# Performance work log

Measured on AMD Instinct MI355X. Metric: run time of the kernel, lower is better.

The kernel has to match this reference:

```python
import jax, jax.numpy as jnp
import numpy as np

B, S, HID, NH, INTER, VOCAB = 8, 1024, 512, 8, 2048, 30522
EPS = 1e-12


def _layernorm(x, w, b):
    m = jnp.mean(x, axis=-1, keepdims=True)
    v = jnp.mean((x - m) ** 2, axis=-1, keepdims=True)
    return (x - m) * jax.lax.rsqrt(v + EPS) * w + b


def _multihead_mut(x, M):
    # x: (b, s, d); M: (H, s, s). Split d into H heads, mix along the
    # sequence axis per head: out[b,t,h,d] = sum_s x[b,s,h,d] * M[h,s,t]
    b, s, d = x.shape
    xh = x.reshape(b, s, NH, d // NH)
    out = jnp.einsum('bshd,hst->bthd', xh, M)
    return out.reshape(b, s, d)


def setup_inputs() -> dict:
    key = jax.random.key(0)
    ks = jax.random.split(key, 14)
    g = lambda i, shape, scale: jax.random.normal(ks[i], shape, dtype=jnp.float32) * scale
    return {
        'x': jax.random.randint(ks[0], (B, S), 0, VOCAB),
        'word_emb': g(1, (VOCAB, HID), 0.02),
        'pos_emb': g(2, (S, HID), 0.02),
        'tok_emb': g(3, (2, HID), 0.02),
        'emb_ln_w': jnp.ones((HID,), dtype=jnp.float32),
        'emb_ln_b': jnp.zeros((HID,), dtype=jnp.float32),
        'init_d': g(4, (INTER, HID), 0.02),
        'init_b': g(5, (INTER,), 0.02),
        'init_M': g(6, (NH, S, S), 1.0 / np.sqrt(S)),
        'inter0_d': g(7, (INTER, INTER), 1.0 / np.sqrt(INTER)),
        'inter0_b': g(8, (INTER,), 0.02),
        'inter0_M': g(9, (NH, S, S), 1.0 / np.sqrt(S)),
        'final_d': g(10, (HID, INTER), 1.0 / np.sqrt(INTER)),
        'final_b': g(11, (HID,), 0.02),
    }


def reference(x, word_emb, pos_emb, tok_emb, emb_ln_w, emb_ln_b,
              init_d, init_b, init_M, inter0_d, inter0_b, inter0_M,
              final_d, final_b):
    # BertEmbeddings: word + position + token_type(all zeros) -> LayerNorm
    emb = word_emb[x] + pos_emb[None, :, :] + tok_emb[0][None, None, :]
    xo = _layernorm(emb, emb_ln_w, emb_ln_b)  # (B, S, HID)

    # layer 0 (flattened): project to intermediate, per-head seq mix, bias, quad act
    xo = xo @ init_d.T                      # (B, S, INTER)
    xo = _multihead_mut(xo, init_M)
    xo = xo + init_b
    xo = xo * xo                            # activation_quad

    # layer 1 (flattened)
    xo = xo @ inter0_d.T                    # (B, S, INTER)
    xo = _multihead_mut(xo, inter0_M)
    xo = xo + inter0_b
    xo = xo * xo                            # activation_quad

    return xo @ final_d.T + final_b         # (B, S, HID)
```

## Files before the change

kernel.cpp:

```cpp
#include <hip/hip_runtime.h>

typedef _Float16 f16;
typedef _Float16 f16x4 __attribute__((ext_vector_type(4)));
typedef _Float16 f16x8 __attribute__((ext_vector_type(8)));
typedef float    f32x4 __attribute__((ext_vector_type(4)));

#define SEQ   1024
#define HID   512
#define NHEAD 8
#define DH    256
#define INTER 2048
#define BATCH 8
#define ROWS  (BATCH * SEQ)

__device__ __forceinline__ void g2l16(const void* g, void* l) {
  __builtin_amdgcn_global_load_lds(
      (const __attribute__((address_space(1))) void*)g,
      (__attribute__((address_space(3))) void*)l, 16, 0, 0);
}

__device__ __forceinline__ void mm_core256(const f16* __restrict__ At,
                                           const f16* __restrict__ Bt,
                                           int K, f32x4 (&acc)[8][4]) {
  __shared__ __align__(16) f16 As[3 * 8192];
  __shared__ __align__(16) f16 Bs[3 * 8192];
  const int tid  = threadIdx.x;
  const int lane = tid & 63, wv = tid >> 6;
  const int wrow = (wv >> 2) * 128, wcol = (wv & 3) * 64;

  const int ch0 = tid, ch1 = tid + 512;
  const int r0 = ch0 >> 2, s0 = ch0 & 3;
  const int r1 = ch1 >> 2, s1 = ch1 & 3;
  const int g0 = r0 * K + ((s0 ^ ((r0 >> 1) & 3)) << 3);
  const int g1 = r1 * K + ((s1 ^ ((r1 >> 1) & 3)) << 3);
  const int l0 = wv * 512;
  const int l1 = 4096 + wv * 512;

  int aoff[8], boff[4];
  const int q = lane >> 4;
  #pragma unroll
  for (int m = 0; m < 8; ++m) {
    int r = wrow + m * 16 + (lane & 15);
    aoff[m] = r * 32 + ((q ^ ((r >> 1) & 3)) << 3);
  }
  #pragma unroll
  for (int n = 0; n < 4; ++n) {
    int r = wcol + n * 16 + (lane & 15);
    boff[n] = r * 32 + ((q ^ ((r >> 1) & 3)) << 3);
  }

  const int nt = K >> 5;
  g2l16(At + g0, &As[l0]);
  g2l16(At + g1, &As[l1]);
  g2l16(Bt + g0, &Bs[l0]);
  g2l16(Bt + g1, &Bs[l1]);
  g2l16(At + 32 + g0, &As[8192 + l0]);
  g2l16(At + 32 + g1, &As[8192 + l1]);
  g2l16(Bt + 32 + g0, &Bs[8192 + l0]);
  g2l16(Bt + 32 + g1, &Bs[8192 + l1]);
  __builtin_amdgcn_sched_barrier(0);
  asm volatile("s_waitcnt vmcnt(4)" ::: "memory");
  __builtin_amdgcn_s_barrier();
  __builtin_amdgcn_sched_barrier(0);

  int slot = 0;
  for (int t = 0; t < nt; ++t) {
    const int cb = slot * 8192;
    const int sb = (slot == 0 ? 2 : slot - 1) * 8192;
    const bool pf = (t + 2 < nt);
    const int kpre = (t + 2) << 5;

    f16x8 bfr[4], af0[4], af1[4];
    #pragma unroll
    for (int n = 0; n < 4; ++n) bfr[n] = *(const f16x8*)&Bs[cb + boff[n]];
    #pragma unroll
    for (int m = 0; m < 4; ++m) af0[m] = *(const f16x8*)&As[cb + aoff[m]];
    if (pf) {
      g2l16(At + kpre + g0, &As[sb + l0]);
      g2l16(At + kpre + g1, &As[sb + l1]);
    }
    __builtin_amdgcn_s_setprio(1);
    #pragma unroll
    for (int m = 0; m < 4; ++m)
      #pragma unroll
      for (int n = 0; n < 4; ++n)
        acc[m][n] = __builtin_amdgcn_mfma_f32_16x16x32_f16(af0[m], bfr[n],
                                                           acc[m][n], 0, 0, 0);
    __builtin_amdgcn_s_setprio(0);
    #pragma unroll
    for (int m = 0; m < 4; ++m) af1[m] = *(const f16x8*)&As[cb + aoff[m + 4]];
    if (pf) {
      g2l16(Bt + kpre + g0, &Bs[sb + l0]);
      g2l16(Bt + kpre + g1, &Bs[sb + l1]);
    }
    __builtin_amdgcn_s_setprio(1);
    #pragma unroll
    for (int m = 0; m < 4; ++m)
      #pragma unroll
      for (int n = 0; n < 4; ++n)
        acc[m + 4][n] = __builtin_amdgcn_mfma_f32_16x16x32_f16(af1[m], bfr[n],
                                                               acc[m + 4][n], 0, 0, 0);
    __builtin_amdgcn_s_setprio(0);
    if (t + 1 < nt) {
      __builtin_amdgcn_sched_barrier(0);
      if (pf) asm volatile("s_waitcnt vmcnt(4)" ::: "memory");
      else    asm volatile("s_waitcnt vmcnt(0)" ::: "memory");
      __builtin_amdgcn_s_barrier();
      __builtin_amdgcn_sched_barrier(0);
    }
    slot = (slot == 2) ? 0 : slot + 1;
  }
}

__device__ __forceinline__ void zero_acc8(f32x4 (&acc)[8][4]) {
  f32x4 z = {0.f, 0.f, 0.f, 0.f};
  #pragma unroll
  for (int i = 0; i < 8; ++i)
    #pragma unroll
    for (int j = 0; j < 4; ++j) acc[i][j] = z;
}

__global__ __launch_bounds__(512, 2) void gemm256_t_kernel(
    const f16* __restrict__ A, const f16* __restrict__ W,
    f16* __restrict__ Xt, int K) {
  int row0 = blockIdx.y * 256, col0 = blockIdx.x * 256;
  f32x4 acc[8][4];
  zero_acc8(acc);
  mm_core256(A + (size_t)row0 * K, W + (size_t)col0 * K, K, acc);
  int tid = threadIdx.x, lane = tid & 63, wv = tid >> 6;
  int wrow = (wv >> 2) * 128, wcol = (wv & 3) * 64;
  int cn = lane & 15, rbase = (lane >> 4) * 4;
  int b = row0 >> 10, sbase = row0 & 1023;
  #pragma unroll
  for (int m = 0; m < 8; ++m) {
    int s = sbase + wrow + m * 16 + rbase;
    #pragma unroll
    for (int n = 0; n < 4; ++n) {
      int col = col0 + wcol + n * 16 + cn;
      int h = col >> 8, d = col & 255;
      f16x4 v = {(f16)acc[m][n][0], (f16)acc[m][n][1],
                 (f16)acc[m][n][2], (f16)acc[m][n][3]};
      *(f16x4*)&Xt[(((size_t)(b * 8 + h) * 256 + d) << 10) + s] = v;
    }
  }
}

__global__ __launch_bounds__(512, 2) void mut256_kernel(
    const f16* __restrict__ Mt, const f16* __restrict__ Xt,
    const float* __restrict__ bias, f16* __restrict__ Y) {
  int b = blockIdx.z >> 3, h = blockIdx.z & 7;
  int t0 = blockIdx.y * 256;
  f32x4 acc[8][4];
  zero_acc8(acc);
  const f16* Ap = Mt + ((size_t)h << 20) + ((size_t)t0 << 10);
  const f16* Bp = Xt + (((size_t)(b * 8 + h)) << 18);
  mm_core256(Ap, Bp, SEQ, acc);
  int tid = threadIdx.x, lane = tid & 63, wv = tid >> 6;
  int wrow = (wv >> 2) * 128, wcol = (wv & 3) * 64;
  int cn = lane & 15, rbase = (lane >> 4) * 4;
  #pragma unroll
  for (int m = 0; m < 8; ++m) {
    int t = t0 + wrow + m * 16 + rbase;
    #pragma unroll
    for (int n = 0; n < 4; ++n) {
      int d = wcol + n * 16 + cn;
      float bb = bias[(h << 8) + d];
      size_t base = (((size_t)(b << 10) + t) << 11) + (h << 8) + d;
      #pragma unroll
      for (int r = 0; r < 4; ++r) {
        float v = acc[m][n][r] + bb;
        Y[base + (size_t)r * INTER] = (f16)(v * v);
      }
    }
  }
}

__device__ __forceinline__ void mm_core(const f16* __restrict__ At,
                                        const f16* __restrict__ Bt,
                                        int K, f32x4 (&acc)[4][4]) {
  __shared__ __align__(16) f16 As[2 * 4096];
  __shared__ __align__(16) f16 Bs[2 * 4096];
  const int tid  = threadIdx.x;
  const int lane = tid & 63, wv = tid >> 6;
  const int wm = (wv >> 1) * 64, wn = (wv & 1) * 64;
  const int lrow  = lane & 15;
  const int kfrag = (lane >> 4) * 8;
  const int c0  = wv * 128 + lane;
  const int r0c = c0 >> 2, q0c = c0 & 3;
  const int c1  = c0 + 64;
  const int r1c = c1 >> 2, q1c = c1 & 3;
  const int ga0 = r0c * K + ((q0c ^ ((r0c >> 1) & 3)) << 3);
  const int ga1 = r1c * K + ((q1c ^ ((r1c >> 1) & 3)) << 3);
  f16* lA0 = &As[wv * 1024];
  f16* lA1 = &As[wv * 1024 + 512];
  f16* lB0 = &Bs[wv * 1024];
  f16* lB1 = &Bs[wv * 1024 + 512];
  int aoff[4], boff[4];
  #pragma unroll
  for (int t = 0; t < 4; ++t) {
    int ra = wm + t * 16 + lrow;
    aoff[t] = ra * 32 + (kfrag ^ (((ra >> 1) & 3) << 3));
    int rb = wn + t * 16 + lrow;
    boff[t] = rb * 32 + (kfrag ^ (((rb >> 1) & 3) << 3));
  }
  g2l16(At + ga0, lA0);
  g2l16(At + ga1, lA1);
  g2l16(Bt + ga0, lB0);
  g2l16(Bt + ga1, lB1);
  __syncthreads();
  int cur = 0;
  for (int k0 = 0; k0 < K; k0 += 32) {
    if (k0 + 32 < K) {
      const int nb = (cur ^ 1) * 4096;
      g2l16(At + (k0 + 32) + ga0, lA0 + nb);
      g2l16(At + (k0 + 32) + ga1, lA1 + nb);
      g2l16(Bt + (k0 + 32) + ga0, lB0 + nb);
      g2l16(Bt + (k0 + 32) + ga1, lB1 + nb);
    }
    const int cb = cur * 4096;
    f16x8 af[4], bf[4];
    #pragma unroll
    for (int t = 0; t < 4; ++t) {
      af[t] = *(const f16x8*)&As[cb + aoff[t]];
      bf[t] = *(const f16x8*)&Bs[cb + boff[t]];
    }
    #pragma unroll
    for (int i = 0; i < 4; ++i)
      #pragma unroll
      for (int j = 0; j < 4; ++j)
        acc[i][j] = __builtin_amdgcn_mfma_f32_16x16x32_f16(af[i], bf[j],
                                                           acc[i][j], 0, 0, 0);
    __syncthreads();
    cur ^= 1;
  }
}

__device__ __forceinline__ void zero_acc(f32x4 (&acc)[4][4]) {
  f32x4 z = {0.f, 0.f, 0.f, 0.f};
  #pragma unroll
  for (int i = 0; i < 4; ++i)
    #pragma unroll
    for (int j = 0; j < 4; ++j) acc[i][j] = z;
}

__global__ __launch_bounds__(256) void gemm_out_kernel(
    const f16* __restrict__ A, const f16* __restrict__ W,
    const float* __restrict__ bias, float* __restrict__ out, int K, int N) {
  int row0 = blockIdx.y * 128, col0 = blockIdx.x * 128;
  f32x4 acc[4][4];
  zero_acc(acc);
  mm_core(A + (size_t)row0 * K, W + (size_t)col0 * K, K, acc);
  int tid = threadIdx.x, lane = tid & 63, wv = tid >> 6;
  int wm = (wv >> 1) * 64, wn = (wv & 1) * 64;
  int cn = lane & 15, rbase = (lane >> 4) * 4;
  #pragma unroll
  for (int mt = 0; mt < 4; ++mt) {
    int r0 = row0 + wm + mt * 16 + rbase;
    #pragma unroll
    for (int nt = 0; nt < 4; ++nt) {
      int col = col0 + wn + nt * 16 + cn;
      float bb = bias[col];
      #pragma unroll
      for (int r = 0; r < 4; ++r)
        out[(size_t)(r0 + r) * N + col] = acc[mt][nt][r] + bb;
    }
  }
}

__global__ __launch_bounds__(256) void embed_ln_kernel(
    const int* __restrict__ x, const float* __restrict__ wemb,
    const float* __restrict__ pemb, const float* __restrict__ temb,
    const float* __restrict__ lnw, const float* __restrict__ lnb,
    f16* __restrict__ out) {
  int row = blockIdx.x;
  int s = row & (SEQ - 1);
  int tok = x[row];
  const float* we = wemb + (size_t)tok * HID;
  const float* pe = pemb + (size_t)s * HID;
  int c = threadIdx.x;
  float e0 = we[c] + pe[c] + temb[c];
  float e1 = we[c + 256] + pe[c + 256] + temb[c + 256];
  float s1 = e0 + e1, s2 = e0 * e0 + e1 * e1;
  #pragma unroll
  for (int off = 32; off > 0; off >>= 1) {
    s1 += __shfl_down(s1, off, 64);
    s2 += __shfl_down(s2, off, 64);
  }
  __shared__ float r1[4], r2[4];
  int wid = threadIdx.x >> 6, lane = threadIdx.x & 63;
  if (lane == 0) { r1[wid] = s1; r2[wid] = s2; }
  __syncthreads();
  float S1 = r1[0] + r1[1] + r1[2] + r1[3];
  float S2 = r2[0] + r2[1] + r2[2] + r2[3];
  float m = S1 * (1.0f / HID);
  float v = S2 * (1.0f / HID) - m * m;
  float inv = rsqrtf(v + 1e-12f);
  f16* o = out + (size_t)row * HID;
  o[c]       = (f16)((e0 - m) * inv * lnw[c]       + lnb[c]);
  o[c + 256] = (f16)((e1 - m) * inv * lnw[c + 256] + lnb[c + 256]);
}

__global__ __launch_bounds__(256) void cast_f16_kernel(
    const float* __restrict__ in, f16* __restrict__ out, int n) {
  int i = (blockIdx.x * 256 + threadIdx.x) * 4;
  if (i < n) {
    float4 v = *(const float4*)(in + i);
    f16x4 o = {(f16)v.x, (f16)v.y, (f16)v.z, (f16)v.w};
    *(f16x4*)(out + i) = o;
  }
}

__global__ __launch_bounds__(256) void mtrans_kernel(
    const float* __restrict__ M, f16* __restrict__ Mt) {
  __shared__ float T[32][33];
  int h = blockIdx.z;
  int s0 = blockIdx.y * 32, t0 = blockIdx.x * 32;
  int tx = threadIdx.x & 31, ty = threadIdx.x >> 5;
  const float* Mh = M + ((size_t)h << 20);
  #pragma unroll
  for (int i = 0; i < 32; i += 8)
    T[ty + i][tx] = Mh[((size_t)(s0 + ty + i) << 10) + t0 + tx];
  __syncthreads();
  f16* Mth = Mt + ((size_t)h << 20);
  #pragma unroll
  for (int i = 0; i < 32; i += 8)
    Mth[((size_t)(t0 + ty + i) << 10) + s0 + tx] = (f16)T[tx][ty + i];
}

extern "C" void kernel_launch(void* const* d_in, const int* in_sizes, int n_in,
                              void* d_out, int out_size, void* d_ws, size_t ws_size,
                              hipStream_t stream) {
  const int*   x        = (const int*)d_in[0];
  const float* wemb     = (const float*)d_in[1];
  const float* pemb     = (const float*)d_in[2];
  const float* temb     = (const float*)d_in[3];
  const float* lnw      = (const float*)d_in[4];
  const float* lnb      = (const float*)d_in[5];
  const float* init_d   = (const float*)d_in[6];
  const float* init_b   = (const float*)d_in[7];
  const float* init_M   = (const float*)d_in[8];
  const float* inter0_d = (const float*)d_in[9];
  const float* inter0_b = (const float*)d_in[10];
  const float* inter0_M = (const float*)d_in[11];
  const float* final_d  = (const float*)d_in[12];
  const float* final_b  = (const float*)d_in[13];
  float* out = (float*)d_out;

  char* ws = (char*)d_ws;
  f16* R0 = (f16*)(ws);
  f16* R1 = (f16*)(ws + 8388608);
  f16* R2 = (f16*)(ws + 10485760);
  f16* R3 = (f16*)(ws + 27262976);
  f16* R4 = (f16*)(ws + 60817408);
  f16* R5 = (f16*)(ws + 94371840);

  embed_ln_kernel<<<ROWS, 256, 0, stream>>>(x, wemb, pemb, temb, lnw, lnb, R0);
  cast_f16_kernel<<<(INTER * HID / 4 + 255) / 256, 256, 0, stream>>>(init_d, R1, INTER * HID);
  mtrans_kernel<<<dim3(32, 32, 8), 256, 0, stream>>>(init_M, R2);
  gemm256_t_kernel<<<dim3(INTER / 256, ROWS / 256), 512, 0, stream>>>(R0, R1, R3, HID);
  mut256_kernel<<<dim3(1, SEQ / 256, BATCH * NHEAD), 512, 0, stream>>>(R2, R3, init_b, R4);
  cast_f16_kernel<<<(INTER * INTER / 4 + 255) / 256, 256, 0, stream>>>(inter0_d, R0, INTER * INTER);
  mtrans_kernel<<<dim3(32, 32, 8), 256, 0, stream>>>(inter0_M, R2);
  gemm256_t_kernel<<<dim3(INTER / 256, ROWS / 256), 512, 0, stream>>>(R4, R0, R5, INTER);
  mut256_kernel<<<dim3(1, SEQ / 256, BATCH * NHEAD), 512, 0, stream>>>(R2, R5, inter0_b, R3);
  cast_f16_kernel<<<(HID * INTER / 4 + 255) / 256, 256, 0, stream>>>(final_d, R1, HID * INTER);
  gemm_out_kernel<<<dim3(HID / 128, ROWS / 128), 256, 0, stream>>>(R3, R1, final_b, out, INTER, HID);
}
```

Measured before the change: 425.4 us.

## Restructure GEMM mainloop to double-buffered K=64 tiles with intra-phase barriers

The shared GEMM core moves from a triple-buffered ring of K=32 slices to two buffers holding K=64 tiles, so each loop iteration runs four MFMA phases over two K=32 halves. Prefetch of the next tile is spread across the four phases, and extra workgroup barriers are placed around each MFMA cluster to keep the waves in lockstep, ping-pong style. The aim is fewer loop-boundary waits and better interleaving of global-to-LDS loads with MFMA. In exchange it uses more LDS per block, which may limit occupancy at two blocks per CU, and adds barrier overhead.

```diff
diff --git a/kernel.cpp b/kernel.cpp
--- a/kernel.cpp
+++ b/kernel.cpp
@@ -19,18 +19,25 @@
       (__attribute__((address_space(3))) void*)l, 16, 0, 0);
 }
 
+#define SYNC_VM4() do { __builtin_amdgcn_sched_barrier(0);            \
+    asm volatile("s_waitcnt vmcnt(4)" ::: "memory");                  \
+    __builtin_amdgcn_s_barrier(); __builtin_amdgcn_sched_barrier(0); } while (0)
+#define SYNC_VM0() do { __builtin_amdgcn_sched_barrier(0);            \
+    asm volatile("s_waitcnt vmcnt(0)" ::: "memory");                  \
+    __builtin_amdgcn_s_barrier(); __builtin_amdgcn_sched_barrier(0); } while (0)
+
 __device__ __forceinline__ void mm_core256(const f16* __restrict__ At,
                                            const f16* __restrict__ Bt,
                                            int K, f32x4 (&acc)[8][4]) {
-  __shared__ __align__(16) f16 As[3 * 8192];
-  __shared__ __align__(16) f16 Bs[3 * 8192];
+  __shared__ __align__(16) f16 As[2 * 16384];
+  __shared__ __align__(16) f16 Bs[2 * 16384];
   const int tid  = threadIdx.x;
   const int lane = tid & 63, wv = tid >> 6;
   const int wrow = (wv >> 2) * 128, wcol = (wv & 3) * 64;
 
-  const int ch0 = tid, ch1 = tid + 512;
-  const int r0 = ch0 >> 2, s0 = ch0 & 3;
-  const int r1 = ch1 >> 2, s1 = ch1 & 3;
+  const int c0 = tid, c1 = tid + 512;
+  const int r0 = c0 >> 2, s0 = c0 & 3;
+  const int r1 = c1 >> 2, s1 = c1 & 3;
   const int g0 = r0 * K + ((s0 ^ ((r0 >> 1) & 3)) << 3);
   const int g1 = r1 * K + ((s1 ^ ((r1 >> 1) & 3)) << 3);
   const int l0 = wv * 512;
@@ -49,7 +56,7 @@
     boff[n] = r * 32 + ((q ^ ((r >> 1) & 3)) << 3);
   }
 
-  const int nt = K >> 5;
+  const int nt = K >> 6;
   g2l16(At + g0, &As[l0]);
   g2l16(At + g1, &As[l1]);
   g2l16(Bt + g0, &Bs[l0]);
@@ -58,57 +65,89 @@
   g2l16(At + 32 + g1, &As[8192 + l1]);
   g2l16(Bt + 32 + g0, &Bs[8192 + l0]);
   g2l16(Bt + 32 + g1, &Bs[8192 + l1]);
-  __builtin_amdgcn_sched_barrier(0);
-  asm volatile("s_waitcnt vmcnt(4)" ::: "memory");
-  __builtin_amdgcn_s_barrier();
-  __builtin_amdgcn_sched_barrier(0);
-
-  int slot = 0;
+  SYNC_VM4();
+
   for (int t = 0; t < nt; ++t) {
-    const int cb = slot * 8192;
-    const int sb = (slot == 0 ? 2 : slot - 1) * 8192;
-    const bool pf = (t + 2 < nt);
-    const int kpre = (t + 2) << 5;
-
-    f16x8 bfr[4], af0[4], af1[4];
-    #pragma unroll
-    for (int n = 0; n < 4; ++n) bfr[n] = *(const f16x8*)&Bs[cb + boff[n]];
-    #pragma unroll
-    for (int m = 0; m < 4; ++m) af0[m] = *(const f16x8*)&As[cb + aoff[m]];
+    const int cb = (t & 1) * 16384;
+    const int nb = ((t + 1) & 1) * 16384;
+    const bool pf = (t + 1 < nt);
+    const int kn = (t + 1) << 6;
+
+    f16x8 b0[4], a0[4];
+    #pragma unroll
+    for (int n = 0; n < 4; ++n) b0[n] = *(const f16x8*)&Bs[cb + boff[n]];
+    #pragma unroll
+    for (int m = 0; m < 4; ++m) a0[m] = *(const f16x8*)&As[cb + aoff[m]];
     if (pf) {
-      g2l16(At + kpre + g0, &As[sb + l0]);
-      g2l16(At + kpre + g1, &As[sb + l1]);
-    }
+      g2l16(At + kn + g0, &As[nb + l0]);
+      g2l16(At + kn + g1, &As[nb + l1]);
+    }
+    __builtin_amdgcn_s_barrier();
     __builtin_amdgcn_s_setprio(1);
     #pragma unroll
     for (int m = 0; m < 4; ++m)
       #pragma unroll
       for (int n = 0; n < 4; ++n)
-        acc[m][n] = __builtin_amdgcn_mfma_f32_16x16x32_f16(af0[m], bfr[n],
+        acc[m][n] = __builtin_amdgcn_mfma_f32_16x16x32_f16(a0[m], b0[n],
                                                            acc[m][n], 0, 0, 0);
     __builtin_amdgcn_s_setprio(0);
-    #pragma unroll
-    for (int m = 0; m < 4; ++m) af1[m] = *(const f16x8*)&As[cb + aoff[m + 4]];
+    __builtin_amdgcn_s_barrier();
+
+    f16x8 a1[4];
+    #pragma unroll
+    for (int m = 0; m < 4; ++m) a1[m] = *(const f16x8*)&As[cb + aoff[m + 4]];
     if (pf) {
-      g2l16(Bt + kpre + g0, &Bs[sb + l0]);
-      g2l16(Bt + kpre + g1, &Bs[sb + l1]);
-    }
+      g2l16(Bt + kn + g0, &Bs[nb + l0]);
+      g2l16(Bt + kn + g1, &Bs[nb + l1]);
+    }
+    __builtin_amdgcn_s_barrier();
     __builtin_amdgcn_s_setprio(1);
     #pragma unroll
     for (int m = 0; m < 4; ++m)
       #pragma unroll
       for (int n = 0; n < 4; ++n)
-        acc[m + 4][n] = __builtin_amdgcn_mfma_f32_16x16x32_f16(af1[m], bfr[n],
+        acc[m + 4][n] = __builtin_amdgcn_mfma_f32_16x16x32_f16(a1[m], b0[n],
                                                                acc[m + 4][n], 0, 0, 0);
     __builtin_amdgcn_s_setprio(0);
-    if (t + 1 < nt) {
-      __builtin_amdgcn_sched_barrier(0);
-      if (pf) asm volatile("s_waitcnt vmcnt(4)" ::: "memory");
-      else    asm volatile("s_waitcnt vmcnt(0)" ::: "memory");
-      __builtin_amdgcn_s_barrier();
-      __builtin_amdgcn_sched_barrier(0);
-    }
-    slot = (slot == 2) ? 0 : slot + 1;
+    if (pf) SYNC_VM4(); else SYNC_VM0();
+
+    f16x8 b1[4], a2[4];
+    #pragma unroll
+    for (int n = 0; n < 4; ++n) b1[n] = *(const f16x8*)&Bs[cb + 8192 + boff[n]];
+    #pragma unroll
+    for (int m = 0; m < 4; ++m) a2[m] = *(const f16x8*)&As[cb + 8192 + aoff[m]];
+    if (pf) {
+      g2l16(At + kn + 32 + g0, &As[nb + 8192 + l0]);
+      g2l16(At + kn + 32 + g1, &As[nb + 8192 + l1]);
+    }
+    __builtin_amdgcn_s_barrier();
+    __builtin_amdgcn_s_setprio(1);
+    #pragma unroll
+    for (int m = 0; m < 4; ++m)
+      #pragma unroll
+      for (int n = 0; n < 4; ++n)
+        acc[m][n] = __builtin_amdgcn_mfma_f32_16x16x32_f16(a2[m], b1[n],
+                                                           acc[m][n], 0, 0, 0);
+    __builtin_amdgcn_s_setprio(0);
+    __builtin_amdgcn_s_barrier();
+
+    f16x8 a3[4];
+    #pragma unroll
+    for (int m = 0; m < 4; ++m) a3[m] = *(const f16x8*)&As[cb + 8192 + aoff[m + 4]];
+    if (pf) {
+      g2l16(Bt + kn + 32 + g0, &Bs[nb + 8192 + l0]);
+      g2l16(Bt + kn + 32 + g1, &Bs[nb + 8192 + l1]);
+    }
+    __builtin_amdgcn_s_barrier();
+    __builtin_amdgcn_s_setprio(1);
+    #pragma unroll
+    for (int m = 0; m < 4; ++m)
+      #pragma unroll
+      for (int n = 0; n < 4; ++n)
+        acc[m + 4][n] = __builtin_amdgcn_mfma_f32_16x16x32_f16(a3[m], b1[n],
+                                                               acc[m + 4][n], 0, 0, 0);
+    __builtin_amdgcn_s_setprio(0);
+    if (pf) SYNC_VM4();
   }
 }
 
```

After: 423.6 us. Within noise of the previous version (-0.4%).

## Deepen GEMM LDS pipeline to four stages with barrier between MFMA halves

Applied to the files above, without the earlier changes.

The shared GEMM core grows its LDS ring from three to four k-slices and prefetches three slices ahead instead of two. All A and B loads for a future slice are now issued together after the second A-fragment read. The wait-and-barrier moves from the end of the iteration to between the two MFMA halves, so the synchronisation overlaps with compute. This aims to hide more global-load latency, at the cost of more LDS per block and the removal of the explicit sched_barriers that fixed instruction order.

```diff
diff --git a/kernel.cpp b/kernel.cpp
--- a/kernel.cpp
+++ b/kernel.cpp
@@ -22,15 +22,15 @@
 __device__ __forceinline__ void mm_core256(const f16* __restrict__ At,
                                            const f16* __restrict__ Bt,
                                            int K, f32x4 (&acc)[8][4]) {
-  __shared__ __align__(16) f16 As[3 * 8192];
-  __shared__ __align__(16) f16 Bs[3 * 8192];
+  __shared__ __align__(16) f16 As[4 * 8192];
+  __shared__ __align__(16) f16 Bs[4 * 8192];
   const int tid  = threadIdx.x;
   const int lane = tid & 63, wv = tid >> 6;
   const int wrow = (wv >> 2) * 128, wcol = (wv & 3) * 64;
 
-  const int ch0 = tid, ch1 = tid + 512;
-  const int r0 = ch0 >> 2, s0 = ch0 & 3;
-  const int r1 = ch1 >> 2, s1 = ch1 & 3;
+  const int c0 = tid, c1 = tid + 512;
+  const int r0 = c0 >> 2, s0 = c0 & 3;
+  const int r1 = c1 >> 2, s1 = c1 & 3;
   const int g0 = r0 * K + ((s0 ^ ((r0 >> 1) & 3)) << 3);
   const int g1 = r1 * K + ((s1 ^ ((r1 >> 1) & 3)) << 3);
   const int l0 = wv * 512;
@@ -50,35 +50,26 @@
   }
 
   const int nt = K >> 5;
-  g2l16(At + g0, &As[l0]);
-  g2l16(At + g1, &As[l1]);
-  g2l16(Bt + g0, &Bs[l0]);
-  g2l16(Bt + g1, &Bs[l1]);
-  g2l16(At + 32 + g0, &As[8192 + l0]);
-  g2l16(At + 32 + g1, &As[8192 + l1]);
-  g2l16(Bt + 32 + g0, &Bs[8192 + l0]);
-  g2l16(Bt + 32 + g1, &Bs[8192 + l1]);
-  __builtin_amdgcn_sched_barrier(0);
-  asm volatile("s_waitcnt vmcnt(4)" ::: "memory");
+  #pragma unroll
+  for (int p = 0; p < 3; ++p) {
+    const int kb = p << 5, sb = p * 8192;
+    g2l16(At + kb + g0, &As[sb + l0]);
+    g2l16(At + kb + g1, &As[sb + l1]);
+    g2l16(Bt + kb + g0, &Bs[sb + l0]);
+    g2l16(Bt + kb + g1, &Bs[sb + l1]);
+  }
+  asm volatile("s_waitcnt vmcnt(8)" ::: "memory");
   __builtin_amdgcn_s_barrier();
-  __builtin_amdgcn_sched_barrier(0);
-
-  int slot = 0;
+
   for (int t = 0; t < nt; ++t) {
-    const int cb = slot * 8192;
-    const int sb = (slot == 0 ? 2 : slot - 1) * 8192;
-    const bool pf = (t + 2 < nt);
-    const int kpre = (t + 2) << 5;
+    const int cb = (t & 3) * 8192;
 
     f16x8 bfr[4], af0[4], af1[4];
     #pragma unroll
     for (int n = 0; n < 4; ++n) bfr[n] = *(const f16x8*)&Bs[cb + boff[n]];
     #pragma unroll
     for (int m = 0; m < 4; ++m) af0[m] = *(const f16x8*)&As[cb + aoff[m]];
-    if (pf) {
-      g2l16(At + kpre + g0, &As[sb + l0]);
-      g2l16(At + kpre + g1, &As[sb + l1]);
-    }
+
     __builtin_amdgcn_s_setprio(1);
     #pragma unroll
     for (int m = 0; m < 4; ++m)
@@ -87,12 +78,25 @@
         acc[m][n] = __builtin_amdgcn_mfma_f32_16x16x32_f16(af0[m], bfr[n],
                                                            acc[m][n], 0, 0, 0);
     __builtin_amdgcn_s_setprio(0);
+
     #pragma unroll
     for (int m = 0; m < 4; ++m) af1[m] = *(const f16x8*)&As[cb + aoff[m + 4]];
-    if (pf) {
-      g2l16(Bt + kpre + g0, &Bs[sb + l0]);
-      g2l16(Bt + kpre + g1, &Bs[sb + l1]);
-    }
+
+    if (t + 3 < nt) {
+      const int kb = (t + 3) << 5, sb = ((t + 3) & 3) * 8192;
+      g2l16(At + kb + g0, &As[sb + l0]);
+      g2l16(At + kb + g1, &As[sb + l1]);
+      g2l16(Bt + kb + g0, &Bs[sb + l0]);
+      g2l16(Bt + kb + g1, &Bs[sb + l1]);
+    }
+
+    if (t + 1 < nt) {
+      if (t + 3 < nt)      asm volatile("s_waitcnt vmcnt(8)" ::: "memory");
+      else if (t + 2 < nt) asm volatile("s_waitcnt vmcnt(4)" ::: "memory");
+      else                 asm volatile("s_waitcnt vmcnt(0)" ::: "memory");
+      __builtin_amdgcn_s_barrier();
+    }
+
     __builtin_amdgcn_s_setprio(1);
     #pragma unroll
     for (int m = 0; m < 4; ++m)
@@ -101,14 +105,6 @@
         acc[m + 4][n] = __builtin_amdgcn_mfma_f32_16x16x32_f16(af1[m], bfr[n],
                                                                acc[m + 4][n], 0, 0, 0);
     __builtin_amdgcn_s_setprio(0);
-    if (t + 1 < nt) {
-      __builtin_amdgcn_sched_barrier(0);
-      if (pf) asm volatile("s_waitcnt vmcnt(4)" ::: "memory");
-      else    asm volatile("s_waitcnt vmcnt(0)" ::: "memory");
-      __builtin_amdgcn_s_barrier();
-      __builtin_amdgcn_sched_barrier(0);
-    }
-    slot = (slot == 2) ? 0 : slot + 1;
   }
 }
 
```

After: 415.8 us. -2.3%, faster.
